# Optimization experiments

Hardware: AMD Instinct MI355X
Metric: run time of the kernel (lower is better)

Reference implementation:

```python
import jax, jax.numpy as jnp
import numpy as np

N = 262144          # ray samples
L = 16              # grid levels
T = 2 ** 19         # hash table entries per level
F = 2               # features per entry
NMIN, NMAX = 16, 2048
SB = 1.0            # scene_bound
DW, CW = 64, 64     # density / color MLP widths

_PRIMES = jnp.array([1, 2654435761, 805459861], dtype=jnp.uint32)
_OFFS = jnp.asarray(np.stack(np.meshgrid([0, 1], [0, 1], [0, 1], indexing='ij'), -1).reshape(8, 3), dtype=jnp.uint32)  # 8 cube corners


def _scalings():
    g = np.exp((np.log(NMAX) - np.log(NMIN)) / (L - 1))
    return jnp.asarray(np.floor(NMIN * g ** np.arange(L)), dtype=jnp.float32)  # (L,)


def hash_encode(pos01, table):
    # pos01: (N,3) in [0,1]; table: (L*T, F)
    scaled = pos01[:, None, :] * _scalings()[None, :, None]        # (N,L,3)
    floor = jnp.floor(scaled)
    frac = scaled - floor                                          # (N,L,3)
    corners = floor.astype(jnp.uint32)[:, :, None, :] + _OFFS[None, None]  # (N,L,8,3)
    h = corners * _PRIMES                                          # uint32 wraparound hashing
    idx = (h[..., 0] ^ h[..., 1] ^ h[..., 2]) % jnp.uint32(T)      # (N,L,8)
    idx = idx.astype(jnp.int32) + (jnp.arange(L, dtype=jnp.int32) * T)[None, :, None]
    feats = table[idx]                                             # (N,L,8,F) gather
    sel = _OFFS.astype(bool)[None, None]                           # (1,1,8,3)
    w = jnp.prod(jnp.where(sel, frac[:, :, None, :], 1.0 - frac[:, :, None, :]), axis=-1)  # (N,L,8)
    out = jnp.einsum('nlcf,nlc->nlf', feats, w)                    # trilinear interp
    return out.reshape(out.shape[0], L * F)                        # (N, 32)


def sh_encode(d):
    # 4th-order real spherical harmonics, 16 components (instant-ngp convention)
    x, y, z = d[..., 0], d[..., 1], d[..., 2]
    xx, yy, zz = x * x, y * y, z * z
    xy, yz, xz = x * y, y * z, x * z
    return jnp.stack([
        jnp.full_like(x, 0.28209479177387814),
        -0.48860251190291987 * y,
        0.48860251190291987 * z,
        -0.48860251190291987 * x,
        1.0925484305920792 * xy,
        -1.0925484305920792 * yz,
        0.94617469575755997 * zz - 0.31539156525252005,
        -1.0925484305920792 * xz,
        0.54627421529603959 * (xx - yy),
        0.59004358992664352 * y * (-3.0 * xx + yy),
        2.8906114426405538 * xy * z,
        0.45704579946446572 * y * (1.0 - 5.0 * zz),
        0.3731763325901154 * z * (5.0 * zz - 3.0),
        0.45704579946446572 * x * (1.0 - 5.0 * zz),
        1.445305721320277 * z * (xx - yy),
        0.59004358992664352 * x * (xx - 3.0 * yy),
    ], axis=-1)  # (N,16)


def setup_inputs() -> dict:
    key = jax.random.key(0)
    ks = jax.random.split(key, 10)
    position = jax.random.uniform(ks[0], (N, 3), jnp.float32, -SB, SB)
    d = jax.random.normal(ks[1], (N, 3), jnp.float32)
    direction = d / jnp.linalg.norm(d, axis=-1, keepdims=True)
    hash_table = jax.random.uniform(ks[2], (L * T, F), jnp.float32, -1e-4, 1e-4)
    def dense(k, fin, fout, std):
        return (jax.random.normal(k, (fin, fout), jnp.float32) * std,
                jnp.zeros((fout,), jnp.float32))
    w1, b1 = dense(ks[3], L * F, DW, 0.01)      # normal() init in source
    w2, b2 = dense(ks[4], DW, 16, 0.01)
    w3, b3 = dense(ks[5], 16 + 16, CW, 0.01)
    w4, b4 = dense(ks[6], CW, CW, 0.01)
    w5, b5 = dense(ks[7], CW, 3, 0.1)           # default lecun-ish scale
    return dict(position=position, direction=direction, hash_table=hash_table,
                w1=w1, b1=b1, w2=w2, b2=b2, w3=w3, b3=b3, w4=w4, b4=b4, w5=w5, b5=b5)


def reference(position, direction, hash_table, w1, b1, w2, b2, w3, b3, w4, b4, w5, b5):
    p = (position + SB) / (2.0 * SB)                 # -> [0,1]
    enc = hash_encode(p, hash_table)                 # (N,32)
    h = jax.nn.relu(enc @ w1 + b1)                   # density MLP
    h = h @ w2 + b2                                  # (N,16)
    density = jnp.exp(h[:, 0:1])                     # exponential_density_activation
    sh = sh_encode(direction)                        # (N,16)
    c = jnp.concatenate([h, sh], axis=-1)            # (N,32)
    c = jax.nn.relu(c @ w3 + b3)
    c = jax.nn.relu(c @ w4 + b4)
    c = c @ w5 + b5
    color = jax.nn.sigmoid(c)                        # high_dynamic_range=False
    return jnp.concatenate([density, color], axis=-1)  # (N,4) drgbs
```

## Files before the change

### kernel.cpp

```cpp
#include <hip/hip_runtime.h>
#include <cmath>

namespace {
constexpr int kN = 262144;
constexpr int kL = 16;
constexpr int kT = 1 << 19;
constexpr unsigned kTMask = kT - 1;

typedef __attribute__((ext_vector_type(8))) short short8;
typedef __attribute__((ext_vector_type(4))) float f32x4;
typedef __attribute__((ext_vector_type(4))) unsigned short ushort4v;

struct Scales { float s[kL]; };

__device__ __forceinline__ unsigned short f2bf(float f) {
    unsigned u = __builtin_bit_cast(unsigned, f);
    return (unsigned short)((u + 0x7FFFu + ((u >> 16) & 1u)) >> 16);
}

__global__ __launch_bounds__(256) void prep_w(
    const float* __restrict__ w1, const float* __restrict__ w2,
    const float* __restrict__ w3, const float* __restrict__ w4,
    const float* __restrict__ w5, unsigned short* __restrict__ out)
{
    const int i = blockIdx.x * 256 + threadIdx.x;
    const int f = i >> 9;
    const int l = (i >> 3) & 63;
    const int e = i & 7;
    const int cl = l & 15;
    const int kg = l >> 4;
    float v = 0.0f;
    if (f < 4) {
        v = w1[(kg * 8 + e) * 64 + f * 16 + cl];
    } else if (f < 6) {
        const int q = f - 4;
        v = w2[(q * 32 + kg * 8 + e) * 16 + cl];
    } else if (f < 10) {
        v = w3[(kg * 8 + e) * 64 + (f - 6) * 16 + cl];
    } else if (f < 18) {
        const int g = f - 10, q = g >> 2, nt = g & 3;
        v = w4[(q * 32 + kg * 8 + e) * 64 + nt * 16 + cl];
    } else {
        const int q = f - 18;
        v = (cl < 3) ? w5[(q * 32 + kg * 8 + e) * 3 + cl] : 0.0f;
    }
    out[i] = f2bf(v);
}

__global__ __launch_bounds__(256) void ngp_encode(
    const float* __restrict__ pos,
    const float2* __restrict__ table,
    unsigned* __restrict__ enc,
    Scales sc)
{
    const int bid = blockIdx.x;
    const int l = bid >> 9;
    const int n0 = ((bid & 511) << 9) | threadIdx.x;

    const float s = sc.s[l];
    const float2* __restrict__ tl = table + (size_t)l * kT;

    float4 pr[2][4];
    float2 ex[2][4];
    unsigned idx0v[2][4];
    unsigned hyzv[2][4];
    unsigned cxv[2];
    float rx[2], ry[2], rz[2];

    #pragma unroll
    for (int t = 0; t < 2; ++t) {
        const int n = n0 + t * 256;
        const float px = (pos[n * 3 + 0] + 1.0f) * 0.5f;
        const float py = (pos[n * 3 + 1] + 1.0f) * 0.5f;
        const float pz = (pos[n * 3 + 2] + 1.0f) * 0.5f;
        const float sx = px * s, sy = py * s, sz = pz * s;
        const float fx = floorf(sx), fy = floorf(sy), fz = floorf(sz);
        rx[t] = sx - fx; ry[t] = sy - fy; rz[t] = sz - fz;
        const unsigned cx = (unsigned)fx, cy = (unsigned)fy, cz = (unsigned)fz;
        cxv[t] = cx;
        const unsigned hy0 = cy * 2654435761u, hy1 = (cy + 1u) * 2654435761u;
        const unsigned hz0 = cz * 805459861u,  hz1 = (cz + 1u) * 805459861u;
        #pragma unroll
        for (int j = 0; j < 4; ++j) {
            const unsigned hyz = ((j >> 1) ? hy1 : hy0) ^ ((j & 1) ? hz1 : hz0);
            hyzv[t][j] = hyz;
            const unsigned idx0 = (cx ^ hyz) & kTMask;
            idx0v[t][j] = idx0;
            pr[t][j] = *reinterpret_cast<const float4*>(tl + (idx0 & ~1u));
        }
    }

    #pragma unroll
    for (int t = 0; t < 2; ++t) {
        if (cxv[t] & 1u) {
            const unsigned cx1 = cxv[t] + 1u;
            #pragma unroll
            for (int j = 0; j < 4; ++j)
                ex[t][j] = tl[(cx1 ^ hyzv[t][j]) & kTMask];
        }
    }

    #pragma unroll
    for (int t = 0; t < 2; ++t) {
        const bool odd = (cxv[t] & 1u) != 0u;
        const float wx0 = 1.0f - rx[t], wx1 = rx[t];
        float f0 = 0.f, f1 = 0.f;
        #pragma unroll
        for (int j = 0; j < 4; ++j) {
            const float wyz = ((j >> 1) ? ry[t] : 1.0f - ry[t]) *
                              ((j & 1) ? rz[t] : 1.0f - rz[t]);
            const bool hi = (idx0v[t][j] & 1u) != 0u;
            const float c0x = hi ? pr[t][j].z : pr[t][j].x;
            const float c0y = hi ? pr[t][j].w : pr[t][j].y;
            const float c1x = odd ? ex[t][j].x : (hi ? pr[t][j].x : pr[t][j].z);
            const float c1y = odd ? ex[t][j].y : (hi ? pr[t][j].y : pr[t][j].w);
            f0 = fmaf(c0x, wx0 * wyz, f0);
            f1 = fmaf(c0y, wx0 * wyz, f1);
            f0 = fmaf(c1x, wx1 * wyz, f0);
            f1 = fmaf(c1y, wx1 * wyz, f1);
        }
        enc[(size_t)l * kN + (n0 + t * 256)] =
            (unsigned)f2bf(f0) | ((unsigned)f2bf(f1) << 16);
    }
}

__global__ __launch_bounds__(256) void ngp_mlp_mfma(
    const unsigned* __restrict__ enc,
    const unsigned short* __restrict__ wbf,
    const float* __restrict__ dir,
    const float* __restrict__ b1, const float* __restrict__ b2,
    const float* __restrict__ b3, const float* __restrict__ b4,
    const float* __restrict__ b5,
    float* __restrict__ out)
{
    __shared__ unsigned short sA[4][4096];
    __shared__ unsigned short sB[4][2048];

    const int tid = threadIdx.x;
    const int wid = tid >> 6;
    const int l   = tid & 63;
    const int cl  = l & 15;
    const int kg  = l >> 4;
    unsigned short* __restrict__ A_ = sA[wid];
    unsigned short* __restrict__ B_ = sB[wid];
    const int gbase = blockIdx.x * 256 + wid * 64;

    {
        const int s = gbase + l;
        const float x = dir[s * 3 + 0], y = dir[s * 3 + 1], z = dir[s * 3 + 2];
        const float xx = x * x, yy = y * y, zz = z * z;
        const float xy = x * y, yz = y * z, xz = x * z;
        float sh[16];
        sh[0] = 0.28209479177387814f;
        sh[1] = -0.48860251190291987f * y;
        sh[2] = 0.48860251190291987f * z;
        sh[3] = -0.48860251190291987f * x;
        sh[4] = 1.0925484305920792f * xy;
        sh[5] = -1.0925484305920792f * yz;
        sh[6] = 0.94617469575755997f * zz - 0.31539156525252005f;
        sh[7] = -1.0925484305920792f * xz;
        sh[8] = 0.54627421529603959f * (xx - yy);
        sh[9] = 0.59004358992664352f * y * (-3.0f * xx + yy);
        sh[10] = 2.8906114426405538f * xy * z;
        sh[11] = 0.45704579946446572f * y * (1.0f - 5.0f * zz);
        sh[12] = 0.3731763325901154f * z * (5.0f * zz - 3.0f);
        sh[13] = 0.45704579946446572f * x * (1.0f - 5.0f * zz);
        sh[14] = 1.445305721320277f * z * (xx - yy);
        sh[15] = 0.59004358992664352f * x * (xx - 3.0f * yy);
        #pragma unroll
        for (int j = 0; j < 16; ++j)
            B_[(l >> 4) * 512 + (16 + j) * 16 + (l & 15)] = f2bf(sh[j]);
    }

    short8 A1[4];
    #pragma unroll
    for (int m = 0; m < 4; ++m) {
        #pragma unroll
        for (int j = 0; j < 4; ++j) {
            const unsigned v = enc[(size_t)(kg * 4 + j) * kN + (gbase + m * 16 + cl)];
            A1[m][2 * j]     = (short)(v & 0xFFFFu);
            A1[m][2 * j + 1] = (short)(v >> 16);
        }
    }
    {
        short8 B1[4];
        #pragma unroll
        for (int nt = 0; nt < 4; ++nt)
            B1[nt] = *reinterpret_cast<const short8*>(&wbf[(size_t)(nt) * 512 + l * 8]);

        f32x4 acc[4][4];
        #pragma unroll
        for (int nt = 0; nt < 4; ++nt) {
            const float bv = b1[nt * 16 + cl];
            #pragma unroll
            for (int m = 0; m < 4; ++m) {
                acc[m][nt][0] = bv; acc[m][nt][1] = bv; acc[m][nt][2] = bv; acc[m][nt][3] = bv;
            }
        }
        #pragma unroll
        for (int m = 0; m < 4; ++m)
            #pragma unroll
            for (int nt = 0; nt < 4; ++nt)
                acc[m][nt] = __builtin_amdgcn_mfma_f32_16x16x32_bf16(A1[m], B1[nt], acc[m][nt], 0, 0, 0);

        #pragma unroll
        for (int m = 0; m < 4; ++m) {
            #pragma unroll
            for (int nt = 0; nt < 4; ++nt) {
                ushort4v pk;
                #pragma unroll
                for (int r = 0; r < 4; ++r) pk[r] = f2bf(fmaxf(acc[m][nt][r], 0.0f));
                *reinterpret_cast<ushort4v*>(&A_[m * 1024 + (nt * 16 + cl) * 16 + kg * 4]) = pk;
            }
        }
    }

    {
        short8 A2[4][2];
        #pragma unroll
        for (int m = 0; m < 4; ++m)
            #pragma unroll
            for (int q = 0; q < 2; ++q)
                #pragma unroll
                for (int e = 0; e < 8; ++e)
                    A2[m][q][e] = (short)A_[m * 1024 + (q * 32 + kg * 8 + e) * 16 + cl];

        short8 B2[2];
        #pragma unroll
        for (int q = 0; q < 2; ++q)
            B2[q] = *reinterpret_cast<const short8*>(&wbf[(size_t)(4 + q) * 512 + l * 8]);

        f32x4 acc[4];
        const float bv = b2[cl];
        #pragma unroll
        for (int m = 0; m < 4; ++m) { acc[m][0] = bv; acc[m][1] = bv; acc[m][2] = bv; acc[m][3] = bv; }
        #pragma unroll
        for (int m = 0; m < 4; ++m)
            #pragma unroll
            for (int q = 0; q < 2; ++q)
                acc[m] = __builtin_amdgcn_mfma_f32_16x16x32_bf16(A2[m][q], B2[q], acc[m], 0, 0, 0);

        #pragma unroll
        for (int m = 0; m < 4; ++m) {
            if (cl == 0) {
                #pragma unroll
                for (int r = 0; r < 4; ++r)
                    out[(size_t)(gbase + m * 16 + kg * 4 + r) * 4 + 0] = expf(acc[m][r]);
            }
            ushort4v pk;
            #pragma unroll
            for (int r = 0; r < 4; ++r) pk[r] = f2bf(acc[m][r]);
            *reinterpret_cast<ushort4v*>(&B_[m * 512 + cl * 16 + kg * 4]) = pk;
        }
    }

    {
        short8 A3[4];
        #pragma unroll
        for (int m = 0; m < 4; ++m)
            #pragma unroll
            for (int e = 0; e < 8; ++e)
                A3[m][e] = (short)B_[m * 512 + (kg * 8 + e) * 16 + cl];

        short8 B3[4];
        #pragma unroll
        for (int nt = 0; nt < 4; ++nt)
            B3[nt] = *reinterpret_cast<const short8*>(&wbf[(size_t)(6 + nt) * 512 + l * 8]);

        f32x4 acc[4][4];
        #pragma unroll
        for (int nt = 0; nt < 4; ++nt) {
            const float bv = b3[nt * 16 + cl];
            #pragma unroll
            for (int m = 0; m < 4; ++m) {
                acc[m][nt][0] = bv; acc[m][nt][1] = bv; acc[m][nt][2] = bv; acc[m][nt][3] = bv;
            }
        }
        #pragma unroll
        for (int m = 0; m < 4; ++m)
            #pragma unroll
            for (int nt = 0; nt < 4; ++nt)
                acc[m][nt] = __builtin_amdgcn_mfma_f32_16x16x32_bf16(A3[m], B3[nt], acc[m][nt], 0, 0, 0);

        #pragma unroll
        for (int m = 0; m < 4; ++m) {
            #pragma unroll
            for (int nt = 0; nt < 4; ++nt) {
                ushort4v pk;
                #pragma unroll
                for (int r = 0; r < 4; ++r) pk[r] = f2bf(fmaxf(acc[m][nt][r], 0.0f));
                *reinterpret_cast<ushort4v*>(&A_[m * 1024 + (nt * 16 + cl) * 16 + kg * 4]) = pk;
            }
        }
    }

    {
        short8 A4[4][2];
        #pragma unroll
        for (int m = 0; m < 4; ++m)
            #pragma unroll
            for (int q = 0; q < 2; ++q)
                #pragma unroll
                for (int e = 0; e < 8; ++e)
                    A4[m][q][e] = (short)A_[m * 1024 + (q * 32 + kg * 8 + e) * 16 + cl];

        short8 B4[2][4];
        #pragma unroll
        for (int q = 0; q < 2; ++q)
            #pragma unroll
            for (int nt = 0; nt < 4; ++nt)
                B4[q][nt] = *reinterpret_cast<const short8*>(&wbf[(size_t)(10 + q * 4 + nt) * 512 + l * 8]);

        f32x4 acc[4][4];
        #pragma unroll
        for (int nt = 0; nt < 4; ++nt) {
            const float bv = b4[nt * 16 + cl];
            #pragma unroll
            for (int m = 0; m < 4; ++m) {
                acc[m][nt][0] = bv; acc[m][nt][1] = bv; acc[m][nt][2] = bv; acc[m][nt][3] = bv;
            }
        }
        #pragma unroll
        for (int m = 0; m < 4; ++m)
            #pragma unroll
            for (int nt = 0; nt < 4; ++nt)
                #pragma unroll
                for (int q = 0; q < 2; ++q)
                    acc[m][nt] = __builtin_amdgcn_mfma_f32_16x16x32_bf16(A4[m][q], B4[q][nt], acc[m][nt], 0, 0, 0);

        #pragma unroll
        for (int m = 0; m < 4; ++m) {
            #pragma unroll
            for (int nt = 0; nt < 4; ++nt) {
                ushort4v pk;
                #pragma unroll
                for (int r = 0; r < 4; ++r) pk[r] = f2bf(fmaxf(acc[m][nt][r], 0.0f));
                *reinterpret_cast<ushort4v*>(&A_[m * 1024 + (nt * 16 + cl) * 16 + kg * 4]) = pk;
            }
        }
    }

    {
        short8 A5[4][2];
        #pragma unroll
        for (int m = 0; m < 4; ++m)
            #pragma unroll
            for (int q = 0; q < 2; ++q)
                #pragma unroll
                for (int e = 0; e < 8; ++e)
                    A5[m][q][e] = (short)A_[m * 1024 + (q * 32 + kg * 8 + e) * 16 + cl];

        short8 B5[2];
        #pragma unroll
        for (int q = 0; q < 2; ++q)
            B5[q] = *reinterpret_cast<const short8*>(&wbf[(size_t)(18 + q) * 512 + l * 8]);

        f32x4 acc[4];
        const float bv = (cl < 3) ? b5[cl] : 0.0f;
        #pragma unroll
        for (int m = 0; m < 4; ++m) { acc[m][0] = bv; acc[m][1] = bv; acc[m][2] = bv; acc[m][3] = bv; }
        #pragma unroll
        for (int m = 0; m < 4; ++m)
            #pragma unroll
            for (int q = 0; q < 2; ++q)
                acc[m] = __builtin_amdgcn_mfma_f32_16x16x32_bf16(A5[m][q], B5[q], acc[m], 0, 0, 0);

        if (cl < 3) {
            #pragma unroll
            for (int m = 0; m < 4; ++m)
                #pragma unroll
                for (int r = 0; r < 4; ++r)
                    out[(size_t)(gbase + m * 16 + kg * 4 + r) * 4 + 1 + cl] =
                        1.0f / (1.0f + expf(-acc[m][r]));
        }
    }
}

}

extern "C" void kernel_launch(void* const* d_in, const int* in_sizes, int n_in,
                              void* d_out, int out_size, void* d_ws, size_t ws_size,
                              hipStream_t stream) {
    (void)in_sizes; (void)n_in; (void)out_size; (void)ws_size;

    Scales sc;
    const double g = exp((log(2048.0) - log(16.0)) / 15.0);
    for (int l = 0; l < kL; ++l) sc.s[l] = (float)floor(16.0 * pow(g, (double)l));

    const float*  pos   = (const float*)d_in[0];
    const float*  dir   = (const float*)d_in[1];
    const float2* table = (const float2*)d_in[2];
    const float *w1 = (const float*)d_in[3],  *b1 = (const float*)d_in[4];
    const float *w2 = (const float*)d_in[5],  *b2 = (const float*)d_in[6];
    const float *w3 = (const float*)d_in[7],  *b3 = (const float*)d_in[8];
    const float *w4 = (const float*)d_in[9],  *b4 = (const float*)d_in[10];
    const float *w5 = (const float*)d_in[11], *b5 = (const float*)d_in[12];
    float* out = (float*)d_out;

    unsigned short* wbf = (unsigned short*)d_ws;
    unsigned* enc = (unsigned*)((char*)d_ws + 32768);

    prep_w<<<40, 256, 0, stream>>>(w1, w2, w3, w4, w5, wbf);
    ngp_encode<<<8192, 256, 0, stream>>>(pos, table, enc, sc);
    ngp_mlp_mfma<<<kN / 256, 256, 0, stream>>>(enc, wbf, dir,
        b1, b2, b3, b4, b5, out);
}
```

Baseline: 151.4 us.

## Fuse hash-grid encoding into MLP kernel, staging features in shared memory

Merges the per-level hash-encoding kernel into the MFMA MLP kernel. Each thread now computes all 16 levels for its own sample, two levels per loop iteration, and writes the bf16 features into a per-wave LDS buffer that then feeds the first MFMA layer. This removes the global write and reread of the encoded feature array and one kernel launch. In exchange the grid shrinks from 8192 to 1024 blocks, so fewer gathers are in flight, and each block touches all 16 level tables instead of one, which may hurt cache locality. The LDS buffers are also merged into one to save space, and the launch-bounds hint now asks for 4 blocks per CU.

```diff
diff --git a/kernel.cpp b/kernel.cpp
--- a/kernel.cpp
+++ b/kernel.cpp
@@ -47,140 +47,129 @@
     out[i] = f2bf(v);
 }
 
-__global__ __launch_bounds__(256) void ngp_encode(
+__global__ __launch_bounds__(256, 4) void ngp_fused(
     const float* __restrict__ pos,
+    const float* __restrict__ dir,
     const float2* __restrict__ table,
-    unsigned* __restrict__ enc,
-    Scales sc)
-{
-    const int bid = blockIdx.x;
-    const int l = bid >> 9;
-    const int n0 = ((bid & 511) << 9) | threadIdx.x;
-
-    const float s = sc.s[l];
-    const float2* __restrict__ tl = table + (size_t)l * kT;
-
-    float4 pr[2][4];
-    float2 ex[2][4];
-    unsigned idx0v[2][4];
-    unsigned hyzv[2][4];
-    unsigned cxv[2];
-    float rx[2], ry[2], rz[2];
-
-    #pragma unroll
-    for (int t = 0; t < 2; ++t) {
-        const int n = n0 + t * 256;
-        const float px = (pos[n * 3 + 0] + 1.0f) * 0.5f;
-        const float py = (pos[n * 3 + 1] + 1.0f) * 0.5f;
-        const float pz = (pos[n * 3 + 2] + 1.0f) * 0.5f;
-        const float sx = px * s, sy = py * s, sz = pz * s;
-        const float fx = floorf(sx), fy = floorf(sy), fz = floorf(sz);
-        rx[t] = sx - fx; ry[t] = sy - fy; rz[t] = sz - fz;
-        const unsigned cx = (unsigned)fx, cy = (unsigned)fy, cz = (unsigned)fz;
-        cxv[t] = cx;
-        const unsigned hy0 = cy * 2654435761u, hy1 = (cy + 1u) * 2654435761u;
-        const unsigned hz0 = cz * 805459861u,  hz1 = (cz + 1u) * 805459861u;
-        #pragma unroll
-        for (int j = 0; j < 4; ++j) {
-            const unsigned hyz = ((j >> 1) ? hy1 : hy0) ^ ((j & 1) ? hz1 : hz0);
-            hyzv[t][j] = hyz;
-            const unsigned idx0 = (cx ^ hyz) & kTMask;
-            idx0v[t][j] = idx0;
-            pr[t][j] = *reinterpret_cast<const float4*>(tl + (idx0 & ~1u));
-        }
-    }
-
-    #pragma unroll
-    for (int t = 0; t < 2; ++t) {
-        if (cxv[t] & 1u) {
-            const unsigned cx1 = cxv[t] + 1u;
-            #pragma unroll
-            for (int j = 0; j < 4; ++j)
-                ex[t][j] = tl[(cx1 ^ hyzv[t][j]) & kTMask];
-        }
-    }
-
-    #pragma unroll
-    for (int t = 0; t < 2; ++t) {
-        const bool odd = (cxv[t] & 1u) != 0u;
-        const float wx0 = 1.0f - rx[t], wx1 = rx[t];
-        float f0 = 0.f, f1 = 0.f;
-        #pragma unroll
-        for (int j = 0; j < 4; ++j) {
-            const float wyz = ((j >> 1) ? ry[t] : 1.0f - ry[t]) *
-                              ((j & 1) ? rz[t] : 1.0f - rz[t]);
-            const bool hi = (idx0v[t][j] & 1u) != 0u;
-            const float c0x = hi ? pr[t][j].z : pr[t][j].x;
-            const float c0y = hi ? pr[t][j].w : pr[t][j].y;
-            const float c1x = odd ? ex[t][j].x : (hi ? pr[t][j].x : pr[t][j].z);
-            const float c1y = odd ? ex[t][j].y : (hi ? pr[t][j].y : pr[t][j].w);
-            f0 = fmaf(c0x, wx0 * wyz, f0);
-            f1 = fmaf(c0y, wx0 * wyz, f1);
-            f0 = fmaf(c1x, wx1 * wyz, f0);
-            f1 = fmaf(c1y, wx1 * wyz, f1);
-        }
-        enc[(size_t)l * kN + (n0 + t * 256)] =
-            (unsigned)f2bf(f0) | ((unsigned)f2bf(f1) << 16);
-    }
-}
-
-__global__ __launch_bounds__(256) void ngp_mlp_mfma(
-    const unsigned* __restrict__ enc,
     const unsigned short* __restrict__ wbf,
-    const float* __restrict__ dir,
     const float* __restrict__ b1, const float* __restrict__ b2,
     const float* __restrict__ b3, const float* __restrict__ b4,
     const float* __restrict__ b5,
-    float* __restrict__ out)
+    float* __restrict__ out, Scales sc)
 {
-    __shared__ unsigned short sA[4][4096];
-    __shared__ unsigned short sB[4][2048];
+    __shared__ unsigned short ubuf[4][4096];
 
     const int tid = threadIdx.x;
     const int wid = tid >> 6;
     const int l   = tid & 63;
     const int cl  = l & 15;
     const int kg  = l >> 4;
-    unsigned short* __restrict__ A_ = sA[wid];
-    unsigned short* __restrict__ B_ = sB[wid];
+    unsigned short* __restrict__ U = ubuf[wid];
+    unsigned* __restrict__ U32 = reinterpret_cast<unsigned*>(U);
+    const int n = blockIdx.x * 256 + tid;
     const int gbase = blockIdx.x * 256 + wid * 64;
 
-    {
-        const int s = gbase + l;
-        const float x = dir[s * 3 + 0], y = dir[s * 3 + 1], z = dir[s * 3 + 2];
-        const float xx = x * x, yy = y * y, zz = z * z;
-        const float xy = x * y, yz = y * z, xz = x * z;
-        float sh[16];
+    const float px = (pos[n * 3 + 0] + 1.0f) * 0.5f;
+    const float py = (pos[n * 3 + 1] + 1.0f) * 0.5f;
+    const float pz = (pos[n * 3 + 2] + 1.0f) * 0.5f;
+    const float dx = dir[n * 3 + 0], dy = dir[n * 3 + 1], dz = dir[n * 3 + 2];
+
+    float sh[16];
+    {
+        const float xx = dx * dx, yy = dy * dy, zz = dz * dz;
+        const float xy = dx * dy, yz = dy * dz, xz = dx * dz;
         sh[0] = 0.28209479177387814f;
-        sh[1] = -0.48860251190291987f * y;
-        sh[2] = 0.48860251190291987f * z;
-        sh[3] = -0.48860251190291987f * x;
+        sh[1] = -0.48860251190291987f * dy;
+        sh[2] = 0.48860251190291987f * dz;
+        sh[3] = -0.48860251190291987f * dx;
         sh[4] = 1.0925484305920792f * xy;
         sh[5] = -1.0925484305920792f * yz;
         sh[6] = 0.94617469575755997f * zz - 0.31539156525252005f;
         sh[7] = -1.0925484305920792f * xz;
         sh[8] = 0.54627421529603959f * (xx - yy);
-        sh[9] = 0.59004358992664352f * y * (-3.0f * xx + yy);
-        sh[10] = 2.8906114426405538f * xy * z;
-        sh[11] = 0.45704579946446572f * y * (1.0f - 5.0f * zz);
-        sh[12] = 0.3731763325901154f * z * (5.0f * zz - 3.0f);
-        sh[13] = 0.45704579946446572f * x * (1.0f - 5.0f * zz);
-        sh[14] = 1.445305721320277f * z * (xx - yy);
-        sh[15] = 0.59004358992664352f * x * (xx - 3.0f * yy);
-        #pragma unroll
-        for (int j = 0; j < 16; ++j)
-            B_[(l >> 4) * 512 + (16 + j) * 16 + (l & 15)] = f2bf(sh[j]);
+        sh[9] = 0.59004358992664352f * dy * (-3.0f * xx + yy);
+        sh[10] = 2.8906114426405538f * xy * dz;
+        sh[11] = 0.45704579946446572f * dy * (1.0f - 5.0f * zz);
+        sh[12] = 0.3731763325901154f * dz * (5.0f * zz - 3.0f);
+        sh[13] = 0.45704579946446572f * dx * (1.0f - 5.0f * zz);
+        sh[14] = 1.445305721320277f * dz * (xx - yy);
+        sh[15] = 0.59004358992664352f * dx * (xx - 3.0f * yy);
+    }
+
+    #pragma unroll 1
+    for (int lg = 0; lg < 8; ++lg) {
+        float4 pr[2][4];
+        float2 ex[2][4];
+        unsigned idx0v[2][4], hyzv[2][4], cxv[2];
+        float rx[2], ry[2], rz[2];
+
+        #pragma unroll
+        for (int t = 0; t < 2; ++t) {
+            const int lv = 2 * lg + t;
+            const float s = sc.s[lv];
+            const float2* __restrict__ tl = table + (size_t)lv * kT;
+            const float sx = px * s, sy = py * s, sz = pz * s;
+            const float fx = floorf(sx), fy = floorf(sy), fz = floorf(sz);
+            rx[t] = sx - fx; ry[t] = sy - fy; rz[t] = sz - fz;
+            const unsigned cx = (unsigned)fx, cy = (unsigned)fy, cz = (unsigned)fz;
+            cxv[t] = cx;
+            const unsigned hy0 = cy * 2654435761u, hy1 = (cy + 1u) * 2654435761u;
+            const unsigned hz0 = cz * 805459861u,  hz1 = (cz + 1u) * 805459861u;
+            #pragma unroll
+            for (int j = 0; j < 4; ++j) {
+                const unsigned hyz = ((j >> 1) ? hy1 : hy0) ^ ((j & 1) ? hz1 : hz0);
+                hyzv[t][j] = hyz;
+                const unsigned idx0 = (cx ^ hyz) & kTMask;
+                idx0v[t][j] = idx0;
+                pr[t][j] = *reinterpret_cast<const float4*>(tl + (idx0 & ~1u));
+            }
+        }
+
+        #pragma unroll
+        for (int t = 0; t < 2; ++t) {
+            if (cxv[t] & 1u) {
+                const int lv = 2 * lg + t;
+                const float2* __restrict__ tl = table + (size_t)lv * kT;
+                const unsigned cx1 = cxv[t] + 1u;
+                #pragma unroll
+                for (int j = 0; j < 4; ++j)
+                    ex[t][j] = tl[(cx1 ^ hyzv[t][j]) & kTMask];
+            }
+        }
+
+        #pragma unroll
+        for (int t = 0; t < 2; ++t) {
+            const bool odd = (cxv[t] & 1u) != 0u;
+            const float wx0 = 1.0f - rx[t], wx1 = rx[t];
+            float f0 = 0.f, f1 = 0.f;
+            #pragma unroll
+            for (int j = 0; j < 4; ++j) {
+                const float wyz = ((j >> 1) ? ry[t] : 1.0f - ry[t]) *
+                                  ((j & 1) ? rz[t] : 1.0f - rz[t]);
+                const bool hi = (idx0v[t][j] & 1u) != 0u;
+                const float c0x = hi ? pr[t][j].z : pr[t][j].x;
+                const float c0y = hi ? pr[t][j].w : pr[t][j].y;
+                const float c1x = odd ? ex[t][j].x : (hi ? pr[t][j].x : pr[t][j].z);
+                const float c1y = odd ? ex[t][j].y : (hi ? pr[t][j].y : pr[t][j].w);
+                f0 = fmaf(c0x, wx0 * wyz, f0);
+                f1 = fmaf(c0y, wx0 * wyz, f1);
+                f0 = fmaf(c1x, wx1 * wyz, f0);
+                f1 = fmaf(c1y, wx1 * wyz, f1);
+            }
+            U32[l * 18 + 2 * lg + t] = (unsigned)f2bf(f0) | ((unsigned)f2bf(f1) << 16);
+        }
     }
 
     short8 A1[4];
     #pragma unroll
     for (int m = 0; m < 4; ++m) {
-        #pragma unroll
-        for (int j = 0; j < 4; ++j) {
-            const unsigned v = enc[(size_t)(kg * 4 + j) * kN + (gbase + m * 16 + cl)];
-            A1[m][2 * j]     = (short)(v & 0xFFFFu);
-            A1[m][2 * j + 1] = (short)(v >> 16);
-        }
+        const int base = (m * 16 + cl) * 18 + kg * 4;
+        const uint2 v01 = *reinterpret_cast<const uint2*>(&U32[base]);
+        const uint2 v23 = *reinterpret_cast<const uint2*>(&U32[base + 2]);
+        A1[m][0] = (short)(v01.x & 0xFFFFu); A1[m][1] = (short)(v01.x >> 16);
+        A1[m][2] = (short)(v01.y & 0xFFFFu); A1[m][3] = (short)(v01.y >> 16);
+        A1[m][4] = (short)(v23.x & 0xFFFFu); A1[m][5] = (short)(v23.x >> 16);
+        A1[m][6] = (short)(v23.y & 0xFFFFu); A1[m][7] = (short)(v23.y >> 16);
     }
     {
         short8 B1[4];
@@ -210,7 +199,7 @@
                 ushort4v pk;
                 #pragma unroll
                 for (int r = 0; r < 4; ++r) pk[r] = f2bf(fmaxf(acc[m][nt][r], 0.0f));
-                *reinterpret_cast<ushort4v*>(&A_[m * 1024 + (nt * 16 + cl) * 16 + kg * 4]) = pk;
+                *reinterpret_cast<ushort4v*>(&U[m * 1024 + (nt * 16 + cl) * 16 + kg * 4]) = pk;
             }
         }
     }
@@ -223,7 +212,7 @@
             for (int q = 0; q < 2; ++q)
                 #pragma unroll
                 for (int e = 0; e < 8; ++e)
-                    A2[m][q][e] = (short)A_[m * 1024 + (q * 32 + kg * 8 + e) * 16 + cl];
+                    A2[m][q][e] = (short)U[m * 1024 + (q * 32 + kg * 8 + e) * 16 + cl];
 
         short8 B2[2];
         #pragma unroll
@@ -250,8 +239,11 @@
             ushort4v pk;
             #pragma unroll
             for (int r = 0; r < 4; ++r) pk[r] = f2bf(acc[m][r]);
-            *reinterpret_cast<ushort4v*>(&B_[m * 512 + cl * 16 + kg * 4]) = pk;
-        }
+            *reinterpret_cast<ushort4v*>(&U[m * 512 + cl * 16 + kg * 4]) = pk;
+        }
+        #pragma unroll
+        for (int j = 0; j < 16; ++j)
+            U[(l >> 4) * 512 + (16 + j) * 16 + (l & 15)] = f2bf(sh[j]);
     }
 
     {
@@ -260,7 +252,7 @@
         for (int m = 0; m < 4; ++m)
             #pragma unroll
             for (int e = 0; e < 8; ++e)
-                A3[m][e] = (short)B_[m * 512 + (kg * 8 + e) * 16 + cl];
+                A3[m][e] = (short)U[m * 512 + (kg * 8 + e) * 16 + cl];
 
         short8 B3[4];
         #pragma unroll
@@ -289,7 +281,7 @@
                 ushort4v pk;
                 #pragma unroll
                 for (int r = 0; r < 4; ++r) pk[r] = f2bf(fmaxf(acc[m][nt][r], 0.0f));
-                *reinterpret_cast<ushort4v*>(&A_[m * 1024 + (nt * 16 + cl) * 16 + kg * 4]) = pk;
+                *reinterpret_cast<ushort4v*>(&U[m * 1024 + (nt * 16 + cl) * 16 + kg * 4]) = pk;
             }
         }
     }
@@ -302,7 +294,7 @@
             for (int q = 0; q < 2; ++q)
                 #pragma unroll
                 for (int e = 0; e < 8; ++e)
-                    A4[m][q][e] = (short)A_[m * 1024 + (q * 32 + kg * 8 + e) * 16 + cl];
+                    A4[m][q][e] = (short)U[m * 1024 + (q * 32 + kg * 8 + e) * 16 + cl];
 
         short8 B4[2][4];
         #pragma unroll
@@ -335,7 +327,7 @@
                 ushort4v pk;
                 #pragma unroll
                 for (int r = 0; r < 4; ++r) pk[r] = f2bf(fmaxf(acc[m][nt][r], 0.0f));
-                *reinterpret_cast<ushort4v*>(&A_[m * 1024 + (nt * 16 + cl) * 16 + kg * 4]) = pk;
+                *reinterpret_cast<ushort4v*>(&U[m * 1024 + (nt * 16 + cl) * 16 + kg * 4]) = pk;
             }
         }
     }
@@ -348,7 +340,7 @@
             for (int q = 0; q < 2; ++q)
                 #pragma unroll
                 for (int e = 0; e < 8; ++e)
-                    A5[m][q][e] = (short)A_[m * 1024 + (q * 32 + kg * 8 + e) * 16 + cl];
+                    A5[m][q][e] = (short)U[m * 1024 + (q * 32 + kg * 8 + e) * 16 + cl];
 
         short8 B5[2];
         #pragma unroll
@@ -398,10 +390,8 @@
     float* out = (float*)d_out;
 
     unsigned short* wbf = (unsigned short*)d_ws;
-    unsigned* enc = (unsigned*)((char*)d_ws + 32768);
 
     prep_w<<<40, 256, 0, stream>>>(w1, w2, w3, w4, w5, wbf);
-    ngp_encode<<<8192, 256, 0, stream>>>(pos, table, enc, sc);
-    ngp_mlp_mfma<<<kN / 256, 256, 0, stream>>>(enc, wbf, dir,
-        b1, b2, b3, b4, b5, out);
-}
+    ngp_fused<<<kN / 256, 256, 0, stream>>>(pos, dir, table, wbf,
+        b1, b2, b3, b4, b5, out, sc);
+}
```

After: 224.6 us. +48.3%, slower.
